# Performance work log

Measured on AMD Instinct MI355X. Metric: run time of the kernel, lower is better.

## Reference

```python
import jax, jax.numpy as jnp
import numpy as np

B_, L_, DM = 8, 1024, 256
DS, DC, EX = 16, 4, 2
DI = EX * DM            # d_inner = 512
DTR = max(1, DM // 16)  # dt_rank = 16


def setup_inputs() -> dict:
    key = jax.random.key(0)
    ks = iter(jax.random.split(key, 40))
    def n(shape, s=0.02):
        return jax.random.normal(next(ks), shape, jnp.float32) * s
    inp = {"x": jax.random.normal(next(ks), (B_, L_, DM), jnp.float32)}
    inp["norm_g"] = jnp.ones((DM,), jnp.float32)
    inp["norm_b"] = jnp.zeros((DM,), jnp.float32)
    for m in ("f", "b"):
        inp[f"inW_{m}"] = n((DM, 2 * DI))
        inp[f"convW_{m}"] = n((DI, DC))
        inp[f"convB_{m}"] = jnp.zeros((DI,), jnp.float32)
        inp[f"xW_{m}"] = n((DI, DTR + 2 * DS))
        inp[f"dtW_{m}"] = n((DTR, DI))
        inp[f"dtB_{m}"] = jnp.zeros((DI,), jnp.float32)
        # ALog init: log of [1..dState] repeated over dInner rows
        inp[f"ALog_{m}"] = jnp.log(jnp.tile(jnp.arange(1, DS + 1, dtype=jnp.float32), (DI, 1)))
        inp[f"Dp_{m}"] = jnp.ones((DI,), jnp.float32)
        inp[f"outW_{m}"] = n((DI, DM))
    inp["fusW"] = n((2 * DM, DM))
    inp["fusB"] = jnp.zeros((DM,), jnp.float32)
    return inp


def _dw_conv(x, w, b):
    # causal depthwise conv1d: x [B,L,DI], w [DI,DC] -> [B,L,DI]
    xc = jnp.transpose(x, (0, 2, 1))  # B,DI,L
    out = jax.lax.conv_general_dilated(
        xc, w[:, None, :], window_strides=(1,), padding=[(DC - 1, 0)],
        dimension_numbers=("NCH", "OIH", "NCH"), feature_group_count=DI)
    return jnp.transpose(out + b[:, None], (0, 2, 1))


def _ssm(x, xW, dtW, dtB, ALog, Dp):
    # x: [B,L,DI]
    A = -jnp.exp(ALog)                                   # [DI,DS]
    xdbl = x @ xW                                        # [B,L,DTR+2*DS]
    dlt, Bp, Cp = jnp.split(xdbl, [DTR, DTR + DS], axis=-1)
    delta = jax.nn.softplus(dlt @ dtW + dtB)             # [B,L,DI]
    dA = jnp.exp(delta[..., None] * A)                   # [B,L,DI,DS]
    dBx = (delta * x)[..., None] * Bp[:, :, None, :]     # [B,L,DI,DS]

    def step(h, t):
        a, bb, c = t
        h = a * h + bb                                   # [B,DI,DS]
        y = jnp.einsum('bdn,bn->bd', h, c)
        return h, y

    h0 = jnp.zeros((x.shape[0], DI, DS), x.dtype)
    _, ys = jax.lax.scan(step, h0, (jnp.moveaxis(dA, 1, 0),
                                    jnp.moveaxis(dBx, 1, 0),
                                    jnp.moveaxis(Cp, 1, 0)))
    return jnp.moveaxis(ys, 0, 1) + Dp * x               # [B,L,DI]


def _mamba(x, inW, convW, convB, xW, dtW, dtB, ALog, Dp, outW):
    xr = x @ inW                                         # [B,L,2*DI]
    xs, res = jnp.split(xr, 2, axis=-1)
    xs = jax.nn.silu(_dw_conv(xs, convW, convB))
    y = _ssm(xs, xW, dtW, dtB, ALog, Dp)
    return (y * jax.nn.silu(res)) @ outW                 # [B,L,DM]


def reference(x, norm_g, norm_b,
              inW_f, convW_f, convB_f, xW_f, dtW_f, dtB_f, ALog_f, Dp_f, outW_f,
              inW_b, convW_b, convB_b, xW_b, dtW_b, dtB_b, ALog_b, Dp_b, outW_b,
              fusW, fusB):
    # LayerNorm
    mu = x.mean(-1, keepdims=True)
    var = ((x - mu) ** 2).mean(-1, keepdims=True)
    xn = (x - mu) * jax.lax.rsqrt(var + 1e-5) * norm_g + norm_b
    # forward-direction Mamba
    xf = _mamba(xn, inW_f, convW_f, convB_f, xW_f, dtW_f, dtB_f, ALog_f, Dp_f, outW_f)
    # backward-direction Mamba (flip along time)
    xb = _mamba(jnp.flip(xn, 1), inW_b, convW_b, convB_b, xW_b, dtW_b, dtB_b, ALog_b, Dp_b, outW_b)
    xb = jnp.flip(xb, 1)
    fused = jnp.concatenate([xf, xb], axis=-1) @ fusW + fusB
    return x + fused  # dropout is identity in eval
```

## Files before the change

kernel.cpp:

```cpp
#include <hip/hip_runtime.h>
#include <cmath>

typedef __bf16 bf16x8 __attribute__((ext_vector_type(8)));
typedef __bf16 bf16x4 __attribute__((ext_vector_type(4)));
typedef float  f32x4  __attribute__((ext_vector_type(4)));
typedef float  f32x2  __attribute__((ext_vector_type(2)));

#define B_  8
#define L_  1024
#define DM  256
#define DI  512
#define DS  16
#define DTR 16
#define M_  (B_*L_)
#define NC  32
#define CT  32

__device__ inline float softplus_f(float z){
  return (z > 20.f) ? z : __logf(1.f + __expf(z));
}
__device__ inline float silu_f(float z){
  return z / (1.f + __expf(-z));
}

__device__ inline int flag_from_x(const void* x){
  const unsigned short* u = (const unsigned short*)x;
  int lane = threadIdx.x & 63;
  unsigned short v = u[2*lane];
  int e = (v >> 7) & 0xFF;
  unsigned long long m = __ballot(e >= 160 || e < 96);
  return __popcll(m) > 16;
}

struct PrepJob { const void* src; void* dst; int rows; int cols; int f32out; };
struct PrepArgs { PrepJob j[26]; int nj; };

__global__ __launch_bounds__(256) void prep_k(PrepArgs a, const void* xsrc){
  const int f = flag_from_x(xsrc);
  int e = blockIdx.x*256 + threadIdx.x;
  #pragma unroll 1
  for (int jj=0; jj<a.nj; jj++){
    int sz = a.j[jj].rows * a.j[jj].cols;
    if (e < sz){
      int cols = a.j[jj].cols;
      int r = e / cols, c = e - r*cols;
      float v = f ? ((const float*)a.j[jj].src)[e] : (float)((const __bf16*)a.j[jj].src)[e];
      if (a.j[jj].f32out) ((float*)a.j[jj].dst)[c*a.j[jj].rows + r] = v;
      else ((__bf16*)a.j[jj].dst)[(long)c*a.j[jj].rows + r] = (__bf16)v;
      return;
    }
    e -= sz;
  }
}

struct TJob { const void* src; __bf16* dst; int R; int C; };
struct TArgs { TJob j[3]; int ntiles[3]; int nj; };

__global__ __launch_bounds__(256) void tpose_k(TArgs a, const void* xsrc){
  const int f = flag_from_x(xsrc);
  __shared__ float tile[64][65];
  int bid = blockIdx.x;
  int jj = 0;
  while (jj < a.nj-1 && bid >= a.ntiles[jj]) { bid -= a.ntiles[jj]; jj++; }
  const TJob J = a.j[jj];
  const int tpr = J.C >> 6;
  const int tr = bid / tpr, tc = bid - tr*tpr;
  const int r0 = tr*64, c0 = tc*64;
  const int tid = threadIdx.x;
  #pragma unroll
  for (int i=0;i<16;i++){
    int idx = i*256 + tid;
    int r = idx >> 6, c = idx & 63;
    long off = (long)(r0+r)*J.C + c0 + c;
    tile[r][c] = f ? ((const float*)J.src)[off] : (float)((const __bf16*)J.src)[off];
  }
  __syncthreads();
  #pragma unroll
  for (int i=0;i<16;i++){
    int idx = i*256 + tid;
    int c = idx >> 6, r = idx & 63;
    J.dst[(long)(c0+c)*J.R + r0 + r] = (__bf16)tile[r][c];
  }
}

__global__ __launch_bounds__(256) void lnw_k(
    const void* x, const __bf16* g, const __bf16* bb, __bf16* xn,
    const __bf16* fusWt, const __bf16* outWr0, const __bf16* outWr1,
    __bf16* BtC0, __bf16* BtC1)
{
  const int bx = blockIdx.x;
  const int tid = threadIdx.x;
  const int lane = tid & 63;
  const int wid = tid >> 6;

  if (bx < M_/4){
    const int f = flag_from_x(x);
    long row = (long)bx*4 + wid;
    long base = row*DM + lane*4;
    float v0,v1,v2,v3;
    if (f){ f32x4 xv = *(const f32x4*)((const float*)x + base);
            v0=xv[0]; v1=xv[1]; v2=xv[2]; v3=xv[3]; }
    else  { bf16x4 xv = *(const bf16x4*)((const __bf16*)x + base);
            v0=(float)xv[0]; v1=(float)xv[1]; v2=(float)xv[2]; v3=(float)xv[3]; }
    float s = v0+v1+v2+v3;
    float q = v0*v0+v1*v1+v2*v2+v3*v3;
    #pragma unroll
    for (int off=32; off>0; off>>=1){ s += __shfl_xor(s,off); q += __shfl_xor(q,off); }
    float mu = s*(1.f/DM), var = q*(1.f/DM)-mu*mu;
    float rs = rsqrtf(var+1e-5f);
    bf16x4 gv = *(const bf16x4*)(g + lane*4);
    bf16x4 bv = *(const bf16x4*)(bb + lane*4);
    bf16x4 o;
    o[0]=(__bf16)((v0-mu)*rs*(float)gv[0]+(float)bv[0]);
    o[1]=(__bf16)((v1-mu)*rs*(float)gv[1]+(float)bv[1]);
    o[2]=(__bf16)((v2-mu)*rs*(float)gv[2]+(float)bv[2]);
    o[3]=(__bf16)((v3-mu)*rs*(float)gv[3]+(float)bv[3]);
    *(bf16x4*)(xn + base) = o;
  } else {
    int b2 = bx - M_/4;
    int wz  = b2 >> 5;
    int rem = b2 & 31;
    int gx = rem & 3, gy = rem >> 2;
    const __bf16* A  = fusWt + wz*DM;
    const __bf16* Bt = wz ? outWr1 : outWr0;
    __bf16* C = wz ? BtC1 : BtC0;
    const int mBase = (gx*4 + wid)*16;
    const int nBase = gy*64;
    const int lm = lane & 15;
    const int kq = (lane >> 4)*8;
    long aoff = (long)(mBase+lm)*(2*DM) + kq;
    long boff[4];
    #pragma unroll
    for (int j=0;j<4;j++) boff[j] = (long)(nBase+j*16+lm)*DM + kq;
    f32x4 acc[4] = {};
    #pragma unroll
    for (int k0=0;k0<DM;k0+=32){
      bf16x8 af = *(const bf16x8*)(A + aoff + k0);
      bf16x8 bfr[4];
      #pragma unroll
      for (int j=0;j<4;j++) bfr[j] = *(const bf16x8*)(Bt + boff[j] + k0);
      #pragma unroll
      for (int j=0;j<4;j++)
        acc[j] = __builtin_amdgcn_mfma_f32_16x16x32_bf16(af, bfr[j], acc[j], 0,0,0);
    }
    #pragma unroll
    for (int rr=0;rr<4;rr++){
      int r = mBase + (lane>>4)*4 + rr;
      #pragma unroll
      for (int j=0;j<4;j++){
        int c = nBase + j*16 + lm;
        C[(long)r*DI + c] = (__bf16)acc[j][rr];
      }
    }
  }
}

template<int BM,int BN,int KK>
__global__ __launch_bounds__(256) void gemm_in_k(
    const __bf16* A, const __bf16* B0, const __bf16* B1,
    __bf16* xz0, __bf16* xz1, __bf16* res0, __bf16* res1,
    int lda, int ldb)
{
  constexpr int TM = BM/2, TN = BN/2;
  constexpr int WMT = TM/16, WNT = TN/16;
  constexpr int LA = BM/64, LB = BN/64;

  const int dir = blockIdx.z;
  const __bf16* Bt = dir ? B1 : B0;
  __bf16* xz  = dir ? xz1 : xz0;
  __bf16* res = dir ? res1 : res0;
  const int tid  = threadIdx.x;
  const int lane = tid & 63;
  const int wid  = tid >> 6;
  const int wm = wid & 1;
  const int wn = wid >> 1;
  const int mBase = blockIdx.x * BM;
  const int nBase = blockIdx.y * BN;
  const int lm = lane & 15;
  const int kq = (lane >> 4) * 8;

  __shared__ __bf16 As[BM*32];
  __shared__ __bf16 Bs[BN*32];

  const __bf16* aS[LA];
  const __bf16* bS[LB];
  {
    int colk = (tid & 3) * 8;
    #pragma unroll
    for (int ld=0; ld<LA; ld++){
      int r = mBase + ld*64 + (tid >> 2);
      if (dir==1){ int b = r >> 10, t = r & (L_-1); r = (b<<10) + (L_-1-t); }
      aS[ld] = A + (long)r*lda + colk;
    }
    #pragma unroll
    for (int ld=0; ld<LB; ld++){
      int r = nBase + ld*64 + (tid >> 2);
      bS[ld] = Bt + (long)r*ldb + colk;
    }
  }

  f32x4 acc[WMT][WNT] = {};
  for (int k0=0; k0<KK; k0+=32){
    #pragma unroll
    for (int ld=0; ld<LA; ld++)
      __builtin_amdgcn_global_load_lds(
        (const __attribute__((address_space(1))) void*)(aS[ld] + k0),
        (__attribute__((address_space(3))) void*)(&As[ld*2048 + tid*8]), 16, 0, 0);
    #pragma unroll
    for (int ld=0; ld<LB; ld++)
      __builtin_amdgcn_global_load_lds(
        (const __attribute__((address_space(1))) void*)(bS[ld] + k0),
        (__attribute__((address_space(3))) void*)(&Bs[ld*2048 + tid*8]), 16, 0, 0);
    __syncthreads();
    bf16x8 af[WMT], bfr[WNT];
    #pragma unroll
    for (int i=0;i<WMT;i++) af[i]  = *(const bf16x8*)&As[(wm*TM + i*16 + lm)*32 + kq];
    #pragma unroll
    for (int j=0;j<WNT;j++) bfr[j] = *(const bf16x8*)&Bs[(wn*TN + j*16 + lm)*32 + kq];
    #pragma unroll
    for (int i=0;i<WMT;i++)
      #pragma unroll
      for (int j=0;j<WNT;j++)
        acc[i][j] = __builtin_amdgcn_mfma_f32_16x16x32_bf16(af[i], bfr[j], acc[i][j], 0,0,0);
    __syncthreads();
  }

  #pragma unroll
  for (int i=0;i<WMT;i++){
    #pragma unroll
    for (int rr=0;rr<4;rr++){
      int r = mBase + wm*TM + i*16 + (lane>>4)*4 + rr;
      #pragma unroll
      for (int j=0;j<WNT;j++){
        int c = nBase + wn*TN + j*16 + lm;
        float v = acc[i][j][rr];
        if (c < DI) xz[(long)r*DI + c] = (__bf16)v;
        else        res[(long)r*DI + (c-DI)] = (__bf16)v;
      }
    }
  }
}

template<int BM,int BN,int KK>
__global__ __launch_bounds__(256) void gemm_fin_k(
    const __bf16* Af, const __bf16* Ab,
    const __bf16* Bt0, const __bf16* Bt1,
    void* Cout, const __bf16* bias, const void* resid)
{
  constexpr int TM = BM/2, TN = BN/2;
  constexpr int WMT = TM/16, WNT = TN/16;
  constexpr int LA = BM/64, LB = BN/64;

  const int of = flag_from_x(resid);
  const int tid  = threadIdx.x;
  const int lane = tid & 63;
  const int wid  = tid >> 6;
  const int wm = wid & 1;
  const int wn = wid >> 1;
  const int mBase = blockIdx.x * BM;
  const int nBase = blockIdx.y * BN;
  const int lm = lane & 15;
  const int kq = (lane >> 4) * 8;

  __shared__ __bf16 As[BM*32];
  __shared__ __bf16 Bs[BN*32];

  f32x4 acc[WMT][WNT] = {};
  #pragma unroll 1
  for (int dd=0; dd<2; dd++){
    const __bf16* A  = dd ? Ab  : Af;
    const __bf16* Bt = dd ? Bt1 : Bt0;
    const __bf16* aS[LA];
    const __bf16* bS[LB];
    {
      int colk = (tid & 3) * 8;
      #pragma unroll
      for (int ld=0; ld<LA; ld++){
        int r = mBase + ld*64 + (tid >> 2);
        if (dd==1){ int b = r >> 10, t = r & (L_-1); r = (b<<10) + (L_-1-t); }
        aS[ld] = A + (long)r*DI + colk;
      }
      #pragma unroll
      for (int ld=0; ld<LB; ld++){
        int r = nBase + ld*64 + (tid >> 2);
        bS[ld] = Bt + (long)r*DI + colk;
      }
    }
    for (int k0=0; k0<KK; k0+=32){
      #pragma unroll
      for (int ld=0; ld<LA; ld++)
        __builtin_amdgcn_global_load_lds(
          (const __attribute__((address_space(1))) void*)(aS[ld] + k0),
          (__attribute__((address_space(3))) void*)(&As[ld*2048 + tid*8]), 16, 0, 0);
      #pragma unroll
      for (int ld=0; ld<LB; ld++)
        __builtin_amdgcn_global_load_lds(
          (const __attribute__((address_space(1))) void*)(bS[ld] + k0),
          (__attribute__((address_space(3))) void*)(&Bs[ld*2048 + tid*8]), 16, 0, 0);
      __syncthreads();
      bf16x8 af[WMT], bfr[WNT];
      #pragma unroll
      for (int i=0;i<WMT;i++) af[i]  = *(const bf16x8*)&As[(wm*TM + i*16 + lm)*32 + kq];
      #pragma unroll
      for (int j=0;j<WNT;j++) bfr[j] = *(const bf16x8*)&Bs[(wn*TN + j*16 + lm)*32 + kq];
      #pragma unroll
      for (int i=0;i<WMT;i++)
        #pragma unroll
        for (int j=0;j<WNT;j++)
          acc[i][j] = __builtin_amdgcn_mfma_f32_16x16x32_bf16(af[i], bfr[j], acc[i][j], 0,0,0);
      __syncthreads();
    }
  }

  #pragma unroll
  for (int i=0;i<WMT;i++){
    #pragma unroll
    for (int rr=0;rr<4;rr++){
      int r = mBase + wm*TM + i*16 + (lane>>4)*4 + rr;
      #pragma unroll
      for (int j=0;j<WNT;j++){
        int c = nBase + wn*TN + j*16 + lm;
        float v = acc[i][j][rr];
        float rsd = of ? ((const float*)resid)[(long)r*DM + c]
                       : (float)((const __bf16*)resid)[(long)r*DM + c];
        v += (float)bias[c] + rsd;
        if (of) ((float*)Cout)[(long)r*DM + c] = v;
        else    ((__bf16*)Cout)[(long)r*DM + c] = (__bf16)v;
      }
    }
  }
}

template<int WMT,int WNT,int BWM,int BWN,int KK>
__global__ __launch_bounds__(64*BWM*BWN) void gemm_r_k(
    const __bf16* A0, const __bf16* A1,
    const __bf16* B0, const __bf16* B1,
    float* C0, float* C1,
    int lda, int ldb, int ldc)
{
  const int dir = blockIdx.z;
  const __bf16* A  = dir ? A1 : A0;
  const __bf16* Bt = dir ? B1 : B0;
  float* C = dir ? C1 : C0;
  const int tid  = threadIdx.x;
  const int lane = tid & 63;
  const int wid  = tid >> 6;
  const int wm = wid % BWM;
  const int wn = wid / BWM;
  const int mBase = (blockIdx.x*BWM + wm) * (WMT*16);
  const int nBase = (blockIdx.y*BWN + wn) * (WNT*16);
  const int lm = lane & 15;
  const int kq = (lane >> 4) * 8;

  long aoff[WMT];
  #pragma unroll
  for (int i=0;i<WMT;i++) aoff[i] = (long)(mBase + i*16 + lm) * lda + kq;
  long boff[WNT];
  #pragma unroll
  for (int j=0;j<WNT;j++) boff[j] = (long)(nBase + j*16 + lm) * ldb + kq;

  f32x4 acc[WMT][WNT] = {};
  #pragma unroll
  for (int k0=0; k0<KK; k0+=32){
    bf16x8 af[WMT], bfr[WNT];
    #pragma unroll
    for (int i=0;i<WMT;i++) af[i]  = *(const bf16x8*)(A  + aoff[i] + k0);
    #pragma unroll
    for (int j=0;j<WNT;j++) bfr[j] = *(const bf16x8*)(Bt + boff[j] + k0);
    #pragma unroll
    for (int i=0;i<WMT;i++)
      #pragma unroll
      for (int j=0;j<WNT;j++)
        acc[i][j] = __builtin_amdgcn_mfma_f32_16x16x32_bf16(af[i], bfr[j], acc[i][j], 0,0,0);
  }

  #pragma unroll
  for (int i=0;i<WMT;i++)
    #pragma unroll
    for (int rr=0;rr<4;rr++){
      int r = mBase + i*16 + (lane>>4)*4 + rr;
      #pragma unroll
      for (int j=0;j<WNT;j++){
        int c = nBase + j*16 + lm;
        C[(long)r*ldc + c] = acc[i][j][rr];
      }
    }
}

__global__ __launch_bounds__(256) void conv_k(
    const __bf16* xz0, const __bf16* xz1,
    const float* cw0, const float* cw1,
    const __bf16* cb0, const __bf16* cb1,
    __bf16* xs0, __bf16* xs1)
{
  const int dir = blockIdx.z;
  const __bf16* xz = dir ? xz1 : xz0;
  const float*  cw = dir ? cw1 : cw0;
  const __bf16* cb = dir ? cb1 : cb0;
  __bf16* xs = dir ? xs1 : xs0;

  int gid = blockIdx.x*256 + threadIdx.x;
  int c8 = gid & 63;
  int t  = (gid >> 6) & (L_-1);
  int b  = gid >> 16;
  int cbase = c8*8;

  float acc[8];
  bf16x8 bb = *(const bf16x8*)(cb + cbase);
  #pragma unroll
  for (int c=0;c<8;c++) acc[c] = (float)bb[c];
  #pragma unroll
  for (int j=0;j<4;j++){
    int tj = t - 3 + j;
    if (tj >= 0){
      bf16x8 xv = *(const bf16x8*)(xz + ((long)(b*L_ + tj))*DI + cbase);
      #pragma unroll
      for (int c=0;c<8;c++) acc[c] += (float)xv[c] * cw[j*DI + cbase + c];
    }
  }
  bf16x8 outv;
  #pragma unroll
  for (int c=0;c<8;c++) outv[c] = (__bf16)silu_f(acc[c]);
  *(bf16x8*)(xs + ((long)(b*L_ + t))*DI + cbase) = outv;
}

__global__ __launch_bounds__(256) void scanA_k(
    const float* xd0, const float* xd1,
    const __bf16* xs0, const __bf16* xs1,
    const float* dw0, const float* dw1,
    const __bf16* dtB0, const __bf16* dtB1,
    const float* ALf0, const float* ALf1,
    float* hend, float* sumd)
{
  const int dir = blockIdx.z;
  const float*  xd  = dir ? xd1 : xd0;
  const __bf16* xs  = dir ? xs1 : xs0;
  const float*  dw  = dir ? dw1 : dw0;
  const __bf16* dtB = dir ? dtB1 : dtB0;
  const float*  ALf = dir ? ALf1 : ALf0;

  const int b   = blockIdx.y;
  const int c   = blockIdx.x >> 1;
  const int dg_ = blockIdx.x & 1;
  const int tid = threadIdx.x;
  const int d   = dg_*256 + tid;
  const int db  = dir*8 + b;
  const long row0 = (long)b*L_ + c*CT;

  __shared__ float sAB[CT][32];
  { int e = tid*4; int t = e>>5, cc = e&31;
    *(f32x4*)&sAB[t][cc] = *(const f32x4*)(xd + (row0+t)*48 + cc); }

  f32x2 dw2[8];
  { const f32x4* p = (const f32x4*)(dw + d*DTR);
    #pragma unroll
    for (int q=0;q<4;q++){ f32x4 v=p[q];
      dw2[q*2]   = f32x2{v[0],v[1]};
      dw2[q*2+1] = f32x2{v[2],v[3]}; } }
  float A[16];
  { const f32x4* p = (const f32x4*)(ALf + d*DS);
    #pragma unroll
    for (int q=0;q<4;q++){ f32x4 v=p[q];
      A[q*4]=-__expf(v[0]); A[q*4+1]=-__expf(v[1]); A[q*4+2]=-__expf(v[2]); A[q*4+3]=-__expf(v[3]); } }
  bool pow_ok = true;
  #pragma unroll
  for (int n=0;n<16;n++) pow_ok = pow_ok && (fabsf(A[n] + (float)(n+1)) < 0.003f*(n+1));
  const float dtbv = (float)dtB[d];

  f32x2 h2[8];
  #pragma unroll
  for (int i=0;i<8;i++) h2[i] = f32x2{0.f,0.f};
  float sdelta = 0.f;
  __syncthreads();

  if (pow_ok){
    #pragma unroll 2
    for (int t=0;t<CT;t++){
      f32x2 z2 = f32x2{dtbv, 0.f};
      #pragma unroll
      for (int i=0;i<8;i++){
        f32x2 qv = *(const f32x2*)&sAB[t][i*2];
        z2 += qv*dw2[i];
      }
      float delta = softplus_f(z2[0]+z2[1]);
      sdelta += delta;
      float xv = (float)xs[(row0+t)*DI + d];
      float dx = delta*xv;
      f32x2 dx2 = f32x2{dx, dx};
      float e1 = __expf(-delta), e2v = e1*e1;
      f32x2 e22 = f32x2{e2v, e2v};
      f32x2 pw = f32x2{e1, e2v};
      #pragma unroll
      for (int i=0;i<8;i++){
        f32x2 Bv = *(const f32x2*)&sAB[t][16+i*2];
        h2[i] = pw*h2[i] + dx2*Bv;
        pw = pw*e22;
      }
    }
  } else {
    #pragma unroll 2
    for (int t=0;t<CT;t++){
      f32x2 z2 = f32x2{dtbv, 0.f};
      #pragma unroll
      for (int i=0;i<8;i++){
        f32x2 qv = *(const f32x2*)&sAB[t][i*2];
        z2 += qv*dw2[i];
      }
      float delta = softplus_f(z2[0]+z2[1]);
      sdelta += delta;
      float xv = (float)xs[(row0+t)*DI + d];
      float dx = delta*xv;
      #pragma unroll
      for (int i=0;i<8;i++){
        f32x2 Bv = *(const f32x2*)&sAB[t][16+i*2];
        f32x2 pw = f32x2{__expf(delta*A[i*2]), __expf(delta*A[i*2+1])};
        h2[i] = pw*h2[i] + f32x2{dx,dx}*Bv;
      }
    }
  }

  long hb = (((long)db*NC + c)*DI + d)*16;
  f32x4* hp = (f32x4*)(hend + hb);
  #pragma unroll
  for (int q=0;q<4;q++){
    f32x4 v; v[0]=h2[q*2][0]; v[1]=h2[q*2][1]; v[2]=h2[q*2+1][0]; v[3]=h2[q*2+1][1];
    hp[q]=v;
  }
  sumd[((long)db*NC + c)*DI + d] = sdelta;
}

__global__ __launch_bounds__(256) void scanB_k(
    const float* ALf0, const float* ALf1,
    const float* hend, const float* sumd, float* Hbuf)
{
  int gid = blockIdx.x*256 + threadIdx.x;
  int n  = gid & 15;
  int d  = (gid>>4) & 511;
  int db = gid >> 13;
  const float* ALf = (db>=8) ? ALf1 : ALf0;
  float A_dn = -__expf(ALf[d*DS + n]);
  float H = 0.f;
  #pragma unroll 1
  for (int c=0;c<NC;c++){
    long base = (((long)db*NC + c)*DI + d)*16 + n;
    Hbuf[base] = H;
    float S = sumd[((long)db*NC + c)*DI + d];
    H = hend[base] + __expf(A_dn*S)*H;
  }
}

__global__ __launch_bounds__(256) void scanC_k(
    const float* xd0, const float* xd1,
    const __bf16* xs0, const __bf16* xs1,
    __bf16* res0, __bf16* res1,
    const float* dw0, const float* dw1,
    const __bf16* dtB0, const __bf16* dtB1,
    const float* ALf0, const float* ALf1,
    const __bf16* Dp0, const __bf16* Dp1,
    const float* Hbuf)
{
  const int dir = blockIdx.z;
  const float*  xd  = dir ? xd1 : xd0;
  const __bf16* xs  = dir ? xs1 : xs0;
  __bf16*       res = dir ? res1 : res0;
  const float*  dw  = dir ? dw1 : dw0;
  const __bf16* dtB = dir ? dtB1 : dtB0;
  const float*  ALf = dir ? ALf1 : ALf0;
  const __bf16* Dp  = dir ? Dp1 : Dp0;

  const int b   = blockIdx.y;
  const int c   = blockIdx.x >> 1;
  const int dg_ = blockIdx.x & 1;
  const int tid = threadIdx.x;
  const int d   = dg_*256 + tid;
  const int db  = dir*8 + b;
  const long row0 = (long)b*L_ + c*CT;

  __shared__ float sX[CT][48];
  for (int v=tid; v<CT*12; v+=256){ int e = v*4; int t = e/48, cc = e - t*48;
    *(f32x4*)&sX[t][cc] = *(const f32x4*)(xd + (row0+t)*48 + cc); }

  f32x2 dw2[8];
  { const f32x4* p = (const f32x4*)(dw + d*DTR);
    #pragma unroll
    for (int q=0;q<4;q++){ f32x4 v=p[q];
      dw2[q*2]   = f32x2{v[0],v[1]};
      dw2[q*2+1] = f32x2{v[2],v[3]}; } }
  float A[16];
  { const f32x4* p = (const f32x4*)(ALf + d*DS);
    #pragma unroll
    for (int q=0;q<4;q++){ f32x4 v=p[q];
      A[q*4]=-__expf(v[0]); A[q*4+1]=-__expf(v[1]); A[q*4+2]=-__expf(v[2]); A[q*4+3]=-__expf(v[3]); } }
  bool pow_ok = true;
  #pragma unroll
  for (int n=0;n<16;n++) pow_ok = pow_ok && (fabsf(A[n] + (float)(n+1)) < 0.003f*(n+1));
  const float dtbv = (float)dtB[d];

  f32x2 h2[8];
  { long hb = (((long)db*NC + c)*DI + d)*16;
    const f32x4* p = (const f32x4*)(Hbuf + hb);
    #pragma unroll
    for (int q=0;q<4;q++){ f32x4 v = p[q];
      h2[q*2]   = f32x2{v[0],v[1]};
      h2[q*2+1] = f32x2{v[2],v[3]}; } }
  const float Dpv = (float)Dp[d];
  __syncthreads();

  if (pow_ok){
    #pragma unroll 2
    for (int t=0;t<CT;t++){
      long row = row0 + t;
      f32x2 z2 = f32x2{dtbv, 0.f};
      #pragma unroll
      for (int i=0;i<8;i++){
        f32x2 qv = *(const f32x2*)&sX[t][i*2];
        z2 += qv*dw2[i];
      }
      float delta = softplus_f(z2[0]+z2[1]);
      float xv = (float)xs[row*DI + d];
      float dx = delta*xv;
      f32x2 dx2 = f32x2{dx, dx};
      float e1 = __expf(-delta), e2v = e1*e1;
      f32x2 e22 = f32x2{e2v, e2v};
      f32x2 pw = f32x2{e1, e2v};
      f32x2 p2 = f32x2{0.f, 0.f};
      #pragma unroll
      for (int i=0;i<8;i++){
        f32x2 Bv = *(const f32x2*)&sX[t][16+i*2];
        f32x2 Cv = *(const f32x2*)&sX[t][32+i*2];
        h2[i] = pw*h2[i] + dx2*Bv;
        p2 += h2[i]*Cv;
        pw = pw*e22;
      }
      float yv = p2[0] + p2[1] + Dpv*xv;
      float rv = (float)res[row*DI + d];
      res[row*DI + d] = (__bf16)(yv * silu_f(rv));
    }
  } else {
    #pragma unroll 2
    for (int t=0;t<CT;t++){
      long row = row0 + t;
      f32x2 z2 = f32x2{dtbv, 0.f};
      #pragma unroll
      for (int i=0;i<8;i++){
        f32x2 qv = *(const f32x2*)&sX[t][i*2];
        z2 += qv*dw2[i];
      }
      float delta = softplus_f(z2[0]+z2[1]);
      float xv = (float)xs[row*DI + d];
      float dx = delta*xv;
      f32x2 p2 = f32x2{0.f, 0.f};
      #pragma unroll
      for (int i=0;i<8;i++){
        f32x2 Bv = *(const f32x2*)&sX[t][16+i*2];
        f32x2 Cv = *(const f32x2*)&sX[t][32+i*2];
        f32x2 pw = f32x2{__expf(delta*A[i*2]), __expf(delta*A[i*2+1])};
        h2[i] = pw*h2[i] + f32x2{dx,dx}*Bv;
        p2 += h2[i]*Cv;
      }
      float yv = p2[0] + p2[1] + Dpv*xv;
      float rv = (float)res[row*DI + d];
      res[row*DI + d] = (__bf16)(yv * silu_f(rv));
    }
  }
}

extern "C" void kernel_launch(void* const* d_in, const int* in_sizes, int n_in,
                              void* d_out, int out_size, void* d_ws, size_t ws_size,
                              hipStream_t stream)
{
  const size_t MB = 1u<<20;
  if (ws_size < 160*MB) return;

  char* w = (char*)d_ws;
  __bf16* xz[2]  = {(__bf16*)(w + 0),      (__bf16*)(w + 8*MB)};
  __bf16* res[2] = {(__bf16*)(w + 16*MB),  (__bf16*)(w + 24*MB)};
  __bf16* xsc[2] = {(__bf16*)(w + 32*MB),  (__bf16*)(w + 40*MB)};
  __bf16* xn     = (__bf16*)(w + 48*MB);
  float*  xdbl[2]= {(float*)(w + 58*MB),   (float*)(w + 58*MB + (size_t)M_*48*4)};

  char* wp = w + 52*MB;
  auto carve = [&](size_t bytes)->void*{
    void* p = wp;
    wp += (bytes + 255) & ~(size_t)255;
    return p;
  };
  __bf16 *inWt[2], *xWt[2], *outWr[2], *BtC[2];
  float *dtWt[2], *convWt[2];
  for (int m=0;m<2;m++){
    inWt[m]   = (__bf16*)carve((size_t)(2*DI)*DM*2);
    xWt[m]    = (__bf16*)carve((size_t)48*DI*2);
    outWr[m]  = (__bf16*)carve((size_t)DI*DM*2);
    BtC[m]    = (__bf16*)carve((size_t)DM*DI*2);
    dtWt[m]   = (float*)carve((size_t)DI*DTR*4);
    convWt[m] = (float*)carve((size_t)4*DI*4);
  }
  __bf16* fusWt = (__bf16*)carve((size_t)DM*(2*DM)*2);
  float* ALf[2] = {(float*)carve((size_t)DI*DS*4), (float*)carve((size_t)DI*DS*4)};

  char* cp = w + 57*MB;
  auto carve2 = [&](size_t elems)->__bf16*{
    __bf16* p = (__bf16*)cp;
    cp += (elems*2 + 255) & ~(size_t)255;
    return p;
  };
  __bf16* ngc = carve2(DM);
  __bf16* nbc = carve2(DM);
  __bf16 *convBc[2], *dtBc[2], *Dpc[2];
  for (int m=0;m<2;m++){
    convBc[m] = carve2(DI);
    dtBc[m]   = carve2(DI);
    Dpc[m]    = carve2(DI);
  }
  __bf16* fusBc = carve2(DM);

  float* hend = (float*)(w + 90*MB);
  float* sumd = (float*)(w + 124*MB);
  float* Hbuf = (float*)(w + 127*MB);

  PrepArgs pa;
  int ji = 0;
  size_t tot = 0;
  auto addj = [&](const void* s, void* dst, int rows, int cols, int f32o){
    pa.j[ji++] = {s, dst, rows, cols, f32o};
    tot += (size_t)rows*cols;
  };
  for (int m=0;m<2;m++){
    int base = 3 + m*9;
    addj(d_in[base+3], xWt[m],   DI,  48,   0);
    addj(d_in[base+8], outWr[m], 1,   DI*DM,0);
    addj(d_in[base+4], dtWt[m],  DTR, DI,   1);
    addj(d_in[base+1], convWt[m],DI,  4,    1);
    addj(d_in[base+2], convBc[m],1, DI, 0);
    addj(d_in[base+5], dtBc[m],  1, DI, 0);
    addj(d_in[base+6], (void*)ALf[m], 1, DI*DS, 1);
    addj(d_in[base+7], Dpc[m],   1, DI, 0);
  }
  addj(d_in[1],  ngc, 1, DM, 0);
  addj(d_in[2],  nbc, 1, DM, 0);
  addj(d_in[22], fusBc, 1, DM, 0);
  pa.nj = ji;
  prep_k<<<(int)((tot+255)/256), 256, 0, stream>>>(pa, d_in[0]);

  TArgs ta;
  ta.j[0] = { d_in[3],  inWt[0], DM,   2*DI }; ta.ntiles[0] = (DM/64)*((2*DI)/64);
  ta.j[1] = { d_in[12], inWt[1], DM,   2*DI }; ta.ntiles[1] = (DM/64)*((2*DI)/64);
  ta.j[2] = { d_in[21], fusWt,   2*DM, DM   }; ta.ntiles[2] = ((2*DM)/64)*(DM/64);
  ta.nj = 3;
  tpose_k<<<ta.ntiles[0]+ta.ntiles[1]+ta.ntiles[2], 256, 0, stream>>>(ta, d_in[0]);

  lnw_k<<<M_/4 + 64, 256, 0, stream>>>(
      d_in[0], ngc, nbc, xn, fusWt, outWr[0], outWr[1], BtC[0], BtC[1]);

  gemm_in_k<128,128,256><<<dim3(M_/128, (2*DI)/128, 2), 256, 0, stream>>>(
      xn, inWt[0], inWt[1], xz[0], xz[1], res[0], res[1], DM, DM);
  conv_k<<<dim3((M_*64)/256, 1, 2), 256, 0, stream>>>(
      xz[0], xz[1], convWt[0], convWt[1], convBc[0], convBc[1], xsc[0], xsc[1]);
  gemm_r_k<1,3,4,1,DI><<<dim3(M_/64, 1, 2), 256, 0, stream>>>(
      xsc[0], xsc[1], xWt[0], xWt[1], xdbl[0], xdbl[1], DI, DI, 48);

  scanA_k<<<dim3(NC*2, B_, 2), 256, 0, stream>>>(
      xdbl[0], xdbl[1], xsc[0], xsc[1], dtWt[0], dtWt[1],
      dtBc[0], dtBc[1], ALf[0], ALf[1], hend, sumd);
  scanB_k<<<131072/256, 256, 0, stream>>>(ALf[0], ALf[1], hend, sumd, Hbuf);
  scanC_k<<<dim3(NC*2, B_, 2), 256, 0, stream>>>(
      xdbl[0], xdbl[1], xsc[0], xsc[1], res[0], res[1],
      dtWt[0], dtWt[1], dtBc[0], dtBc[1], ALf[0], ALf[1], Dpc[0], Dpc[1], Hbuf);

  gemm_fin_k<64,64,DI><<<dim3(M_/64, DM/64, 1), 256, 0, stream>>>(
      res[0], res[1], BtC[0], BtC[1], d_out, fusBc, d_in[0]);
}
```

Before: 251.6 us.

## Fuse depthwise conv and x-projection GEMM into both scan chunk kernels

Removes the standalone conv and x_proj GEMM kernels. Each scan chunk block now recomputes the causal conv+SiLU for its 32 timesteps into swizzled LDS and runs the 48-wide projection with MFMA, in both scanA and scanC. This drops the global round trips for xs and xdbl and two launches. The cost is doing the conv/GEMM work twice, plus 512-thread blocks with a larger LDS footprint. The weight prep and transpose kernels are also merged into one launch, and scanB preloads its chunk values into registers.

```diff
diff --git a/kernel.cpp b/kernel.cpp
--- a/kernel.cpp
+++ b/kernel.cpp
@@ -34,52 +34,50 @@
 
 struct PrepJob { const void* src; void* dst; int rows; int cols; int f32out; };
 struct PrepArgs { PrepJob j[26]; int nj; };
-
-__global__ __launch_bounds__(256) void prep_k(PrepArgs a, const void* xsrc){
+struct TJob { const void* src; __bf16* dst; int R; int C; };
+struct TArgs { TJob j[3]; int ntiles[3]; int nj; int ntot; };
+
+__global__ __launch_bounds__(256) void wprep_k(TArgs ta, PrepArgs a, const void* xsrc){
   const int f = flag_from_x(xsrc);
-  int e = blockIdx.x*256 + threadIdx.x;
-  #pragma unroll 1
-  for (int jj=0; jj<a.nj; jj++){
-    int sz = a.j[jj].rows * a.j[jj].cols;
-    if (e < sz){
-      int cols = a.j[jj].cols;
-      int r = e / cols, c = e - r*cols;
-      float v = f ? ((const float*)a.j[jj].src)[e] : (float)((const __bf16*)a.j[jj].src)[e];
-      if (a.j[jj].f32out) ((float*)a.j[jj].dst)[c*a.j[jj].rows + r] = v;
-      else ((__bf16*)a.j[jj].dst)[(long)c*a.j[jj].rows + r] = (__bf16)v;
-      return;
-    }
-    e -= sz;
-  }
-}
-
-struct TJob { const void* src; __bf16* dst; int R; int C; };
-struct TArgs { TJob j[3]; int ntiles[3]; int nj; };
-
-__global__ __launch_bounds__(256) void tpose_k(TArgs a, const void* xsrc){
-  const int f = flag_from_x(xsrc);
-  __shared__ float tile[64][65];
-  int bid = blockIdx.x;
-  int jj = 0;
-  while (jj < a.nj-1 && bid >= a.ntiles[jj]) { bid -= a.ntiles[jj]; jj++; }
-  const TJob J = a.j[jj];
-  const int tpr = J.C >> 6;
-  const int tr = bid / tpr, tc = bid - tr*tpr;
-  const int r0 = tr*64, c0 = tc*64;
   const int tid = threadIdx.x;
-  #pragma unroll
-  for (int i=0;i<16;i++){
-    int idx = i*256 + tid;
-    int r = idx >> 6, c = idx & 63;
-    long off = (long)(r0+r)*J.C + c0 + c;
-    tile[r][c] = f ? ((const float*)J.src)[off] : (float)((const __bf16*)J.src)[off];
-  }
-  __syncthreads();
-  #pragma unroll
-  for (int i=0;i<16;i++){
-    int idx = i*256 + tid;
-    int c = idx >> 6, r = idx & 63;
-    J.dst[(long)(c0+c)*J.R + r0 + r] = (__bf16)tile[r][c];
+  if ((int)blockIdx.x < ta.ntot){
+    __shared__ float tile[64][65];
+    int bid = blockIdx.x;
+    int jj = 0;
+    while (jj < ta.nj-1 && bid >= ta.ntiles[jj]) { bid -= ta.ntiles[jj]; jj++; }
+    const TJob J = ta.j[jj];
+    const int tpr = J.C >> 6;
+    const int tr = bid / tpr, tc = bid - tr*tpr;
+    const int r0 = tr*64, c0 = tc*64;
+    #pragma unroll
+    for (int i=0;i<16;i++){
+      int idx = i*256 + tid;
+      int r = idx >> 6, c = idx & 63;
+      long off = (long)(r0+r)*J.C + c0 + c;
+      tile[r][c] = f ? ((const float*)J.src)[off] : (float)((const __bf16*)J.src)[off];
+    }
+    __syncthreads();
+    #pragma unroll
+    for (int i=0;i<16;i++){
+      int idx = i*256 + tid;
+      int c = idx >> 6, r = idx & 63;
+      J.dst[(long)(c0+c)*J.R + r0 + r] = (__bf16)tile[r][c];
+    }
+  } else {
+    int e = (blockIdx.x - ta.ntot)*256 + tid;
+    #pragma unroll 1
+    for (int jj=0; jj<a.nj; jj++){
+      int sz = a.j[jj].rows * a.j[jj].cols;
+      if (e < sz){
+        int cols = a.j[jj].cols;
+        int r = e / cols, c = e - r*cols;
+        float v = f ? ((const float*)a.j[jj].src)[e] : (float)((const __bf16*)a.j[jj].src)[e];
+        if (a.j[jj].f32out) ((float*)a.j[jj].dst)[c*a.j[jj].rows + r] = v;
+        else ((__bf16*)a.j[jj].dst)[(long)c*a.j[jj].rows + r] = (__bf16)v;
+        return;
+      }
+      e -= sz;
+    }
   }
 }
 
@@ -331,125 +329,78 @@
   }
 }
 
-template<int WMT,int WNT,int BWM,int BWN,int KK>
-__global__ __launch_bounds__(64*BWM*BWN) void gemm_r_k(
-    const __bf16* A0, const __bf16* A1,
-    const __bf16* B0, const __bf16* B1,
-    float* C0, float* C1,
-    int lda, int ldb, int ldc)
-{
-  const int dir = blockIdx.z;
-  const __bf16* A  = dir ? A1 : A0;
-  const __bf16* Bt = dir ? B1 : B0;
-  float* C = dir ? C1 : C0;
-  const int tid  = threadIdx.x;
-  const int lane = tid & 63;
-  const int wid  = tid >> 6;
-  const int wm = wid % BWM;
-  const int wn = wid / BWM;
-  const int mBase = (blockIdx.x*BWM + wm) * (WMT*16);
-  const int nBase = (blockIdx.y*BWN + wn) * (WNT*16);
-  const int lm = lane & 15;
-  const int kq = (lane >> 4) * 8;
-
-  long aoff[WMT];
-  #pragma unroll
-  for (int i=0;i<WMT;i++) aoff[i] = (long)(mBase + i*16 + lm) * lda + kq;
-  long boff[WNT];
-  #pragma unroll
-  for (int j=0;j<WNT;j++) boff[j] = (long)(nBase + j*16 + lm) * ldb + kq;
-
-  f32x4 acc[WMT][WNT] = {};
-  #pragma unroll
-  for (int k0=0; k0<KK; k0+=32){
-    bf16x8 af[WMT], bfr[WNT];
-    #pragma unroll
-    for (int i=0;i<WMT;i++) af[i]  = *(const bf16x8*)(A  + aoff[i] + k0);
-    #pragma unroll
-    for (int j=0;j<WNT;j++) bfr[j] = *(const bf16x8*)(Bt + boff[j] + k0);
-    #pragma unroll
-    for (int i=0;i<WMT;i++)
-      #pragma unroll
-      for (int j=0;j<WNT;j++)
-        acc[i][j] = __builtin_amdgcn_mfma_f32_16x16x32_bf16(af[i], bfr[j], acc[i][j], 0,0,0);
-  }
-
-  #pragma unroll
-  for (int i=0;i<WMT;i++)
-    #pragma unroll
-    for (int rr=0;rr<4;rr++){
-      int r = mBase + i*16 + (lane>>4)*4 + rr;
-      #pragma unroll
-      for (int j=0;j<WNT;j++){
-        int c = nBase + j*16 + lm;
-        C[(long)r*ldc + c] = acc[i][j][rr];
-      }
-    }
-}
-
-__global__ __launch_bounds__(256) void conv_k(
+__global__ __launch_bounds__(512) void scanA_k(
     const __bf16* xz0, const __bf16* xz1,
     const float* cw0, const float* cw1,
     const __bf16* cb0, const __bf16* cb1,
-    __bf16* xs0, __bf16* xs1)
-{
-  const int dir = blockIdx.z;
-  const __bf16* xz = dir ? xz1 : xz0;
-  const float*  cw = dir ? cw1 : cw0;
-  const __bf16* cb = dir ? cb1 : cb0;
-  __bf16* xs = dir ? xs1 : xs0;
-
-  int gid = blockIdx.x*256 + threadIdx.x;
-  int c8 = gid & 63;
-  int t  = (gid >> 6) & (L_-1);
-  int b  = gid >> 16;
-  int cbase = c8*8;
-
-  float acc[8];
-  bf16x8 bb = *(const bf16x8*)(cb + cbase);
-  #pragma unroll
-  for (int c=0;c<8;c++) acc[c] = (float)bb[c];
-  #pragma unroll
-  for (int j=0;j<4;j++){
-    int tj = t - 3 + j;
-    if (tj >= 0){
-      bf16x8 xv = *(const bf16x8*)(xz + ((long)(b*L_ + tj))*DI + cbase);
-      #pragma unroll
-      for (int c=0;c<8;c++) acc[c] += (float)xv[c] * cw[j*DI + cbase + c];
-    }
-  }
-  bf16x8 outv;
-  #pragma unroll
-  for (int c=0;c<8;c++) outv[c] = (__bf16)silu_f(acc[c]);
-  *(bf16x8*)(xs + ((long)(b*L_ + t))*DI + cbase) = outv;
-}
-
-__global__ __launch_bounds__(256) void scanA_k(
-    const float* xd0, const float* xd1,
-    const __bf16* xs0, const __bf16* xs1,
+    const __bf16* xW0, const __bf16* xW1,
     const float* dw0, const float* dw1,
     const __bf16* dtB0, const __bf16* dtB1,
     const float* ALf0, const float* ALf1,
     float* hend, float* sumd)
 {
   const int dir = blockIdx.z;
-  const float*  xd  = dir ? xd1 : xd0;
-  const __bf16* xs  = dir ? xs1 : xs0;
+  const __bf16* xz  = dir ? xz1 : xz0;
+  const float*  cw  = dir ? cw1 : cw0;
+  const __bf16* cb  = dir ? cb1 : cb0;
+  const __bf16* xWt = dir ? xW1 : xW0;
   const float*  dw  = dir ? dw1 : dw0;
   const __bf16* dtB = dir ? dtB1 : dtB0;
   const float*  ALf = dir ? ALf1 : ALf0;
 
   const int b   = blockIdx.y;
-  const int c   = blockIdx.x >> 1;
-  const int dg_ = blockIdx.x & 1;
+  const int c   = blockIdx.x;
   const int tid = threadIdx.x;
-  const int d   = dg_*256 + tid;
+  const int lane = tid & 63;
+  const int wid  = tid >> 6;
+  const int d   = tid;
   const int db  = dir*8 + b;
   const long row0 = (long)b*L_ + c*CT;
 
-  __shared__ float sAB[CT][32];
-  { int e = tid*4; int t = e>>5, cc = e&31;
-    *(f32x4*)&sAB[t][cc] = *(const f32x4*)(xd + (row0+t)*48 + cc); }
+  __shared__ __bf16 xs_s[CT*DI];
+  __shared__ float  sX[CT][48];
+
+  {
+    const float c0 = cw[0*DI+d], c1 = cw[1*DI+d], c2 = cw[2*DI+d], c3 = cw[3*DI+d];
+    const float cbv = (float)cb[d];
+    int gt0 = c*CT;
+    float xm3 = (gt0-3 >= 0) ? (float)xz[(row0-3)*DI + d] : 0.f;
+    float xm2 = (gt0-2 >= 0) ? (float)xz[(row0-2)*DI + d] : 0.f;
+    float xm1 = (gt0-1 >= 0) ? (float)xz[(row0-1)*DI + d] : 0.f;
+    #pragma unroll 8
+    for (int t=0;t<CT;t++){
+      float xt = (float)xz[(row0+t)*DI + d];
+      float a = cbv;
+      a += xm3*c0; a += xm2*c1; a += xm1*c2; a += xt*c3;
+      float sv = silu_f(a);
+      *(__bf16*)((char*)xs_s + t*1024 + ((2*d) ^ ((t&7)<<4))) = (__bf16)sv;
+      xm3 = xm2; xm2 = xm1; xm1 = xt;
+    }
+  }
+  __syncthreads();
+
+  if (wid < 6){
+    const int mb = (wid & 1) * 16;
+    const int nb = (wid >> 1) * 16;
+    const int lm = lane & 15;
+    const int kq = (lane >> 4) * 8;
+    const int row = mb + lm;
+    const char* abase = (const char*)xs_s + row*1024;
+    const int rsw = (row&7)<<4;
+    const __bf16* Bt = xWt + (long)(nb + lm)*DI + kq;
+    f32x4 acc = {};
+    #pragma unroll
+    for (int k0=0;k0<DI;k0+=32){
+      bf16x8 af  = *(const bf16x8*)(abase + (((kq + k0)*2) ^ rsw));
+      bf16x8 bfr = *(const bf16x8*)(Bt + k0);
+      acc = __builtin_amdgcn_mfma_f32_16x16x32_bf16(af, bfr, acc, 0,0,0);
+    }
+    #pragma unroll
+    for (int rr=0;rr<4;rr++){
+      int r = mb + (lane>>4)*4 + rr;
+      sX[r][nb + lm] = acc[rr];
+    }
+  }
 
   f32x2 dw2[8];
   { const f32x4* p = (const f32x4*)(dw + d*DTR);
@@ -479,12 +430,12 @@
       f32x2 z2 = f32x2{dtbv, 0.f};
       #pragma unroll
       for (int i=0;i<8;i++){
-        f32x2 qv = *(const f32x2*)&sAB[t][i*2];
+        f32x2 qv = *(const f32x2*)&sX[t][i*2];
         z2 += qv*dw2[i];
       }
       float delta = softplus_f(z2[0]+z2[1]);
       sdelta += delta;
-      float xv = (float)xs[(row0+t)*DI + d];
+      float xv = (float)*(const __bf16*)((const char*)xs_s + t*1024 + ((2*d) ^ ((t&7)<<4)));
       float dx = delta*xv;
       f32x2 dx2 = f32x2{dx, dx};
       float e1 = __expf(-delta), e2v = e1*e1;
@@ -492,7 +443,7 @@
       f32x2 pw = f32x2{e1, e2v};
       #pragma unroll
       for (int i=0;i<8;i++){
-        f32x2 Bv = *(const f32x2*)&sAB[t][16+i*2];
+        f32x2 Bv = *(const f32x2*)&sX[t][16+i*2];
         h2[i] = pw*h2[i] + dx2*Bv;
         pw = pw*e22;
       }
@@ -503,16 +454,16 @@
       f32x2 z2 = f32x2{dtbv, 0.f};
       #pragma unroll
       for (int i=0;i<8;i++){
-        f32x2 qv = *(const f32x2*)&sAB[t][i*2];
+        f32x2 qv = *(const f32x2*)&sX[t][i*2];
         z2 += qv*dw2[i];
       }
       float delta = softplus_f(z2[0]+z2[1]);
       sdelta += delta;
-      float xv = (float)xs[(row0+t)*DI + d];
+      float xv = (float)*(const __bf16*)((const char*)xs_s + t*1024 + ((2*d) ^ ((t&7)<<4)));
       float dx = delta*xv;
       #pragma unroll
       for (int i=0;i<8;i++){
-        f32x2 Bv = *(const f32x2*)&sAB[t][16+i*2];
+        f32x2 Bv = *(const f32x2*)&sX[t][16+i*2];
         f32x2 pw = f32x2{__expf(delta*A[i*2]), __expf(delta*A[i*2+1])};
         h2[i] = pw*h2[i] + f32x2{dx,dx}*Bv;
       }
@@ -539,19 +490,27 @@
   int db = gid >> 13;
   const float* ALf = (db>=8) ? ALf1 : ALf0;
   float A_dn = -__expf(ALf[d*DS + n]);
+  const long base0 = (((long)db*NC)*DI + d)*16 + n;
+  const long cstr  = (long)DI*16;
+  const long sbase = (long)db*NC*DI + d;
+  float he[NC], Sv[NC];
+  #pragma unroll
+  for (int c=0;c<NC;c++) he[c] = hend[base0 + c*cstr];
+  #pragma unroll
+  for (int c=0;c<NC;c++) Sv[c] = sumd[sbase + c*DI];
   float H = 0.f;
-  #pragma unroll 1
+  #pragma unroll
   for (int c=0;c<NC;c++){
-    long base = (((long)db*NC + c)*DI + d)*16 + n;
-    Hbuf[base] = H;
-    float S = sumd[((long)db*NC + c)*DI + d];
-    H = hend[base] + __expf(A_dn*S)*H;
-  }
-}
-
-__global__ __launch_bounds__(256) void scanC_k(
-    const float* xd0, const float* xd1,
-    const __bf16* xs0, const __bf16* xs1,
+    Hbuf[base0 + c*cstr] = H;
+    H = he[c] + __expf(A_dn*Sv[c])*H;
+  }
+}
+
+__global__ __launch_bounds__(512) void scanC_k(
+    const __bf16* xz0, const __bf16* xz1,
+    const float* cw0, const float* cw1,
+    const __bf16* cb0, const __bf16* cb1,
+    const __bf16* xW0, const __bf16* xW1,
     __bf16* res0, __bf16* res1,
     const float* dw0, const float* dw1,
     const __bf16* dtB0, const __bf16* dtB1,
@@ -560,8 +519,10 @@
     const float* Hbuf)
 {
   const int dir = blockIdx.z;
-  const float*  xd  = dir ? xd1 : xd0;
-  const __bf16* xs  = dir ? xs1 : xs0;
+  const __bf16* xz  = dir ? xz1 : xz0;
+  const float*  cw  = dir ? cw1 : cw0;
+  const __bf16* cb  = dir ? cb1 : cb0;
+  const __bf16* xWt = dir ? xW1 : xW0;
   __bf16*       res = dir ? res1 : res0;
   const float*  dw  = dir ? dw1 : dw0;
   const __bf16* dtB = dir ? dtB1 : dtB0;
@@ -569,16 +530,58 @@
   const __bf16* Dp  = dir ? Dp1 : Dp0;
 
   const int b   = blockIdx.y;
-  const int c   = blockIdx.x >> 1;
-  const int dg_ = blockIdx.x & 1;
+  const int c   = blockIdx.x;
   const int tid = threadIdx.x;
-  const int d   = dg_*256 + tid;
+  const int lane = tid & 63;
+  const int wid  = tid >> 6;
+  const int d   = tid;
   const int db  = dir*8 + b;
   const long row0 = (long)b*L_ + c*CT;
 
-  __shared__ float sX[CT][48];
-  for (int v=tid; v<CT*12; v+=256){ int e = v*4; int t = e/48, cc = e - t*48;
-    *(f32x4*)&sX[t][cc] = *(const f32x4*)(xd + (row0+t)*48 + cc); }
+  __shared__ __bf16 xs_s[CT*DI];
+  __shared__ float  sX[CT][48];
+
+  {
+    const float c0 = cw[0*DI+d], c1 = cw[1*DI+d], c2 = cw[2*DI+d], c3 = cw[3*DI+d];
+    const float cbv = (float)cb[d];
+    int gt0 = c*CT;
+    float xm3 = (gt0-3 >= 0) ? (float)xz[(row0-3)*DI + d] : 0.f;
+    float xm2 = (gt0-2 >= 0) ? (float)xz[(row0-2)*DI + d] : 0.f;
+    float xm1 = (gt0-1 >= 0) ? (float)xz[(row0-1)*DI + d] : 0.f;
+    #pragma unroll 8
+    for (int t=0;t<CT;t++){
+      float xt = (float)xz[(row0+t)*DI + d];
+      float a = cbv;
+      a += xm3*c0; a += xm2*c1; a += xm1*c2; a += xt*c3;
+      float sv = silu_f(a);
+      *(__bf16*)((char*)xs_s + t*1024 + ((2*d) ^ ((t&7)<<4))) = (__bf16)sv;
+      xm3 = xm2; xm2 = xm1; xm1 = xt;
+    }
+  }
+  __syncthreads();
+
+  if (wid < 6){
+    const int mb = (wid & 1) * 16;
+    const int nb = (wid >> 1) * 16;
+    const int lm = lane & 15;
+    const int kq = (lane >> 4) * 8;
+    const int row = mb + lm;
+    const char* abase = (const char*)xs_s + row*1024;
+    const int rsw = (row&7)<<4;
+    const __bf16* Bt = xWt + (long)(nb + lm)*DI + kq;
+    f32x4 acc = {};
+    #pragma unroll
+    for (int k0=0;k0<DI;k0+=32){
+      bf16x8 af  = *(const bf16x8*)(abase + (((kq + k0)*2) ^ rsw));
+      bf16x8 bfr = *(const bf16x8*)(Bt + k0);
+      acc = __builtin_amdgcn_mfma_f32_16x16x32_bf16(af, bfr, acc, 0,0,0);
+    }
+    #pragma unroll
+    for (int rr=0;rr<4;rr++){
+      int r = mb + (lane>>4)*4 + rr;
+      sX[r][nb + lm] = acc[rr];
+    }
+  }
 
   f32x2 dw2[8];
   { const f32x4* p = (const f32x4*)(dw + d*DTR);
@@ -617,7 +620,7 @@
         z2 += qv*dw2[i];
       }
       float delta = softplus_f(z2[0]+z2[1]);
-      float xv = (float)xs[row*DI + d];
+      float xv = (float)*(const __bf16*)((const char*)xs_s + t*1024 + ((2*d) ^ ((t&7)<<4)));
       float dx = delta*xv;
       f32x2 dx2 = f32x2{dx, dx};
       float e1 = __expf(-delta), e2v = e1*e1;
@@ -647,7 +650,7 @@
         z2 += qv*dw2[i];
       }
       float delta = softplus_f(z2[0]+z2[1]);
-      float xv = (float)xs[row*DI + d];
+      float xv = (float)*(const __bf16*)((const char*)xs_s + t*1024 + ((2*d) ^ ((t&7)<<4)));
       float dx = delta*xv;
       f32x2 p2 = f32x2{0.f, 0.f};
       #pragma unroll
@@ -675,9 +678,7 @@
   char* w = (char*)d_ws;
   __bf16* xz[2]  = {(__bf16*)(w + 0),      (__bf16*)(w + 8*MB)};
   __bf16* res[2] = {(__bf16*)(w + 16*MB),  (__bf16*)(w + 24*MB)};
-  __bf16* xsc[2] = {(__bf16*)(w + 32*MB),  (__bf16*)(w + 40*MB)};
   __bf16* xn     = (__bf16*)(w + 48*MB);
-  float*  xdbl[2]= {(float*)(w + 58*MB),   (float*)(w + 58*MB + (size_t)M_*48*4)};
 
   char* wp = w + 52*MB;
   auto carve = [&](size_t bytes)->void*{
@@ -740,31 +741,30 @@
   addj(d_in[2],  nbc, 1, DM, 0);
   addj(d_in[22], fusBc, 1, DM, 0);
   pa.nj = ji;
-  prep_k<<<(int)((tot+255)/256), 256, 0, stream>>>(pa, d_in[0]);
 
   TArgs ta;
   ta.j[0] = { d_in[3],  inWt[0], DM,   2*DI }; ta.ntiles[0] = (DM/64)*((2*DI)/64);
   ta.j[1] = { d_in[12], inWt[1], DM,   2*DI }; ta.ntiles[1] = (DM/64)*((2*DI)/64);
   ta.j[2] = { d_in[21], fusWt,   2*DM, DM   }; ta.ntiles[2] = ((2*DM)/64)*(DM/64);
   ta.nj = 3;
-  tpose_k<<<ta.ntiles[0]+ta.ntiles[1]+ta.ntiles[2], 256, 0, stream>>>(ta, d_in[0]);
+  ta.ntot = ta.ntiles[0]+ta.ntiles[1]+ta.ntiles[2];
+  int prepBlocks = (int)((tot+255)/256);
+  wprep_k<<<ta.ntot + prepBlocks, 256, 0, stream>>>(ta, pa, d_in[0]);
 
   lnw_k<<<M_/4 + 64, 256, 0, stream>>>(
       d_in[0], ngc, nbc, xn, fusWt, outWr[0], outWr[1], BtC[0], BtC[1]);
 
   gemm_in_k<128,128,256><<<dim3(M_/128, (2*DI)/128, 2), 256, 0, stream>>>(
       xn, inWt[0], inWt[1], xz[0], xz[1], res[0], res[1], DM, DM);
-  conv_k<<<dim3((M_*64)/256, 1, 2), 256, 0, stream>>>(
-      xz[0], xz[1], convWt[0], convWt[1], convBc[0], convBc[1], xsc[0], xsc[1]);
-  gemm_r_k<1,3,4,1,DI><<<dim3(M_/64, 1, 2), 256, 0, stream>>>(
-      xsc[0], xsc[1], xWt[0], xWt[1], xdbl[0], xdbl[1], DI, DI, 48);
-
-  scanA_k<<<dim3(NC*2, B_, 2), 256, 0, stream>>>(
-      xdbl[0], xdbl[1], xsc[0], xsc[1], dtWt[0], dtWt[1],
+
+  scanA_k<<<dim3(NC, B_, 2), 512, 0, stream>>>(
+      xz[0], xz[1], convWt[0], convWt[1], convBc[0], convBc[1],
+      xWt[0], xWt[1], dtWt[0], dtWt[1],
       dtBc[0], dtBc[1], ALf[0], ALf[1], hend, sumd);
   scanB_k<<<131072/256, 256, 0, stream>>>(ALf[0], ALf[1], hend, sumd, Hbuf);
-  scanC_k<<<dim3(NC*2, B_, 2), 256, 0, stream>>>(
-      xdbl[0], xdbl[1], xsc[0], xsc[1], res[0], res[1],
+  scanC_k<<<dim3(NC, B_, 2), 512, 0, stream>>>(
+      xz[0], xz[1], convWt[0], convWt[1], convBc[0], convBc[1],
+      xWt[0], xWt[1], res[0], res[1],
       dtWt[0], dtWt[1], dtBc[0], dtBc[1], ALf[0], ALf[1], Dpc[0], Dpc[1], Hbuf);
 
   gemm_fin_k<64,64,DI><<<dim3(M_/64, DM/64, 1), 256, 0, stream>>>(
```

Measured after the change: 236.4 us. 1.06x faster.
